# Kernel optimization log

Measured on AMD Instinct MI355X. Metric: run time of the kernel, lower is better.

The kernel has to match this reference:

```python
import jax, jax.numpy as jnp
import numpy as np

D_MODEL = 1024
D_MEMORY = 768
NUM_HEADS = 16
HEAD_DIM = D_MODEL // NUM_HEADS


def _linear_params(key, d_in, d_out):
    kw, kb = jax.random.split(key)
    bound = 1.0 / np.sqrt(d_in)
    W = jax.random.uniform(kw, (d_out, d_in), jnp.float32, -bound, bound)
    b = jax.random.uniform(kb, (d_out,), jnp.float32, -bound, bound)
    return W, b


def setup_inputs() -> dict:
    key = jax.random.key(0)
    ks = jax.random.split(key, 9)
    B, S, M = 2, 2048, 4096
    query = jax.random.normal(ks[0], (B, S, D_MODEL), jnp.float32)
    memory_keys = jax.random.normal(ks[1], (B, M, D_MEMORY), jnp.float32)
    memory_values = jax.random.normal(ks[2], (B, M, D_MEMORY), jnp.float32)
    Wq, bq = _linear_params(ks[3], D_MODEL, D_MODEL)
    Wk, bk = _linear_params(ks[4], D_MEMORY, D_MODEL)
    Wv, bv = _linear_params(ks[5], D_MEMORY, D_MODEL)
    Wo, bo = _linear_params(ks[6], D_MODEL, D_MODEL)
    Wg1, bg1 = _linear_params(ks[7], 2 * D_MODEL, D_MODEL)
    Wg2, bg2 = _linear_params(ks[8], D_MODEL, 1)
    return dict(query=query, memory_keys=memory_keys, memory_values=memory_values,
                Wq=Wq, bq=bq, Wk=Wk, bk=bk, Wv=Wv, bv=bv, Wo=Wo, bo=bo,
                Wg1=Wg1, bg1=bg1, Wg2=Wg2, bg2=bg2)


def reference(query, memory_keys, memory_values,
              Wq, bq, Wk, bk, Wv, bv, Wo, bo, Wg1, bg1, Wg2, bg2):
    B, S, _ = query.shape
    M = memory_keys.shape[1]
    H, Dh = NUM_HEADS, HEAD_DIM
    # projections (torch Linear: x @ W.T + b)
    Q = (query @ Wq.T + bq).reshape(B, S, H, Dh)
    K = (memory_keys @ Wk.T + bk).reshape(B, M, H, Dh)
    V = (memory_values @ Wv.T + bv).reshape(B, M, H, Dh)
    scale = Dh ** -0.5
    attn = jnp.einsum('bshd,bmhd->bhsm', Q, K) * scale
    attn = jax.nn.softmax(attn, axis=-1)
    retrieved = jnp.einsum('bhsm,bmhd->bshd', attn, V).reshape(B, S, H * Dh)
    retrieved = retrieved @ Wo.T + bo
    # gate: Linear -> SiLU -> Linear -> Sigmoid on [query; retrieved]
    g = jnp.concatenate([query, retrieved], axis=-1) @ Wg1.T + bg1
    g = jax.nn.silu(g)
    gate = jax.nn.sigmoid(g @ Wg2.T + bg2)  # [B,S,1]
    return query + gate * retrieved
```

## Files before the change

### kernel.cpp

```cpp
#include <hip/hip_runtime.h>

typedef __attribute__((ext_vector_type(8))) __bf16 bf16x8;
typedef __attribute__((ext_vector_type(4))) float f32x4;
typedef __attribute__((ext_vector_type(16))) float f32x16;
typedef __attribute__((ext_vector_type(8))) unsigned short u16x8;
typedef __attribute__((ext_vector_type(4))) unsigned u32x4;

__device__ __forceinline__ ushort f2bf(float x) {
    unsigned u = __builtin_bit_cast(unsigned, x);
    unsigned r = u + 0x7fffu + ((u >> 16) & 1u);
    return (ushort)(r >> 16);
}
__device__ __forceinline__ float bf2f(ushort u) {
    unsigned v = ((unsigned)u) << 16;
    return __builtin_bit_cast(float, v);
}

__device__ __forceinline__ unsigned cvtpk(float lo, float hi) {
    unsigned r;
    asm("v_cvt_pk_bf16_f32 %0, %1, %2" : "=v"(r) : "v"(lo), "v"(hi));
    return r;
}

__device__ __forceinline__ void gload16(const void* g, void* l) {
    __builtin_amdgcn_global_load_lds(
        (const __attribute__((address_space(1))) void*)g,
        (__attribute__((address_space(3))) void*)l,
        16, 0, 0);
}

#define MFMA16(a, b, cIn) __builtin_amdgcn_mfma_f32_16x16x32_bf16((a), (b), (cIn), 0, 0, 0)
#define MFMA32(a, b, cIn) __builtin_amdgcn_mfma_f32_32x32x16_bf16((a), (b), (cIn), 0, 0, 0)

__device__ __forceinline__ bf16x8 pv_frag(unsigned ua, unsigned ub, unsigned uc, unsigned ud) {
    unsigned x1 = ua, y1 = uc, x2 = ub, y2 = ud;
    asm("v_permlane32_swap_b32 %0, %1" : "+v"(x1), "+v"(y1));
    asm("v_permlane32_swap_b32 %0, %1" : "+v"(x2), "+v"(y2));
    u32x4 wv; wv[0] = x1; wv[1] = x2; wv[2] = y1; wv[3] = y2;
    return __builtin_bit_cast(bf16x8, wv);
}

__global__ __launch_bounds__(256) void cvt_kv(const float* __restrict__ a, ushort* __restrict__ ab,
                                              const float* __restrict__ bsrc, ushort* __restrict__ bb,
                                              int n4) {
    const int stride = gridDim.x * 256;
    for (int i = blockIdx.x * 256 + threadIdx.x; i < n4; i += stride) {
        float4 v = ((const float4*)a)[i];
        ushort4 o; o.x = f2bf(v.x); o.y = f2bf(v.y); o.z = f2bf(v.z); o.w = f2bf(v.w);
        ((ushort4*)ab)[i] = o;
    }
    for (int i = blockIdx.x * 256 + threadIdx.x; i < n4; i += stride) {
        float4 v = ((const float4*)bsrc)[i];
        ushort4 o; o.x = f2bf(v.x); o.y = f2bf(v.y); o.z = f2bf(v.z); o.w = f2bf(v.w);
        ((ushort4*)bb)[i] = o;
    }
}

__global__ __launch_bounds__(256) void cvt_weights(
    const float* __restrict__ s0, ushort* __restrict__ d0, int n0,
    const float* __restrict__ s1, ushort* __restrict__ d1, int n1,
    const float* __restrict__ s2, ushort* __restrict__ d2, int n2,
    const float* __restrict__ s3, ushort* __restrict__ d3, int n3,
    const float* __restrict__ s4, ushort* __restrict__ d4, int n4c) {
    const int stride = gridDim.x * 256;
    const int t0 = blockIdx.x * 256 + threadIdx.x;
#define CVT_SEG(S, D, N)                                                  \
    for (int i = t0; i < (N); i += stride) {                              \
        float4 v = ((const float4*)(S))[i];                               \
        ushort4 o; o.x = f2bf(v.x); o.y = f2bf(v.y);                      \
        o.z = f2bf(v.z); o.w = f2bf(v.w);                                 \
        ((ushort4*)(D))[i] = o;                                           \
    }
    CVT_SEG(s0, d0, n0) CVT_SEG(s1, d1, n1) CVT_SEG(s2, d2, n2)
    CVT_SEG(s3, d3, n3) CVT_SEG(s4, d4, n4c)
#undef CVT_SEG
}

__global__ __launch_bounds__(256) void cvt_query_cat(const float* __restrict__ in,
                                                     ushort* __restrict__ cat) {
    const int r = blockIdx.x, t = threadIdx.x;
    float4 v = ((const float4*)(in + (size_t)r * 1024))[t];
    ushort4 o;
    o.x = f2bf(v.x); o.y = f2bf(v.y); o.z = f2bf(v.z); o.w = f2bf(v.w);
    ((ushort4*)(cat + (size_t)r * 2048))[t] = o;
}

template<int EPI>
__global__ __launch_bounds__(256, 2) void gemm_bt(
    const ushort* __restrict__ A, int lda,
    const ushort* __restrict__ Bw, int ldb,
    const float* __restrict__ bias,
    ushort* __restrict__ o_bf, int ld0,
    float* __restrict__ o_f32,
    int K, float scale)
{
    __shared__ __align__(1024) char smem[65536];
    const int t = threadIdx.x, w = t >> 6, l = t & 63, g = l >> 4, c = l & 15;
    const int wr = w >> 1, wc = w & 1;
    const long m0 = (long)blockIdx.y * 128, n0 = (long)blockIdx.x * 128;
    const size_t ldaB = (size_t)lda * 2, ldbB = (size_t)ldb * 2;
    const int swz = (c & 7) << 4;
    const int o0 = w * 1024 + l * 16;

    auto gsrc = [&](const char* base, size_t ldB, long r0, int o) {
        const int row = o >> 7, cb = o & 127;
        return base + (size_t)(r0 + row) * ldB + (cb ^ ((row & 7) << 4));
    };
    const char* aP0 = gsrc((const char*)A, ldaB, m0, o0);
    const char* aP1 = gsrc((const char*)A, ldaB, m0, o0 + 4096);
    const char* aP2 = gsrc((const char*)A, ldaB, m0, o0 + 8192);
    const char* aP3 = gsrc((const char*)A, ldaB, m0, o0 + 12288);
    const char* bP0 = gsrc((const char*)Bw, ldbB, n0, o0);
    const char* bP1 = gsrc((const char*)Bw, ldbB, n0, o0 + 4096);
    const char* bP2 = gsrc((const char*)Bw, ldbB, n0, o0 + 8192);
    const char* bP3 = gsrc((const char*)Bw, ldbB, n0, o0 + 12288);

    const int aRd0 = (wr * 64 + c) * 128 + ((g * 16) ^ swz);
    const int aRd1 = aRd0 ^ 64;
    const int bRd0 = 32768 + (wc * 64 + c) * 128 + ((g * 16) ^ swz);
    const int bRd1 = bRd0 ^ 64;

    f32x4 acc[4][4];
#pragma unroll
    for (int i = 0; i < 4; ++i)
#pragma unroll
        for (int j = 0; j < 4; ++j) acc[i][j] = (f32x4)0.0f;

    auto stage = [&](int slot) {
        char* Ab = smem + slot * 16384;
        char* Bb = smem + 32768 + slot * 16384;
        gload16(aP0, Ab + w * 1024);
        gload16(aP1, Ab + 4096 + w * 1024);
        gload16(aP2, Ab + 8192 + w * 1024);
        gload16(aP3, Ab + 12288 + w * 1024);
        gload16(bP0, Bb + w * 1024);
        gload16(bP1, Bb + 4096 + w * 1024);
        gload16(bP2, Bb + 8192 + w * 1024);
        gload16(bP3, Bb + 12288 + w * 1024);
        aP0 += 128; aP1 += 128; aP2 += 128; aP3 += 128;
        bP0 += 128; bP1 += 128; bP2 += 128; bP3 += 128;
    };

    const int nkt = K >> 6;
    stage(0);
    for (int kt = 0; kt < nkt; ++kt) {
        const bool pf = (kt + 1 < nkt);
        if (pf) {
            stage((kt + 1) & 1);
            asm volatile("s_waitcnt vmcnt(8)" ::: "memory");
        } else {
            asm volatile("s_waitcnt vmcnt(0)" ::: "memory");
        }
        __builtin_amdgcn_s_barrier();
        const char* Ac = smem + (kt & 1) * 16384;
        const char* Bc = smem + (kt & 1) * 16384;
#pragma unroll
        for (int kf = 0; kf < 2; ++kf) {
            const int ar = kf ? aRd1 : aRd0, br = kf ? bRd1 : bRd0;
            bf16x8 af0 = *(const bf16x8*)(Ac + 0 + ar);
            bf16x8 af1 = *(const bf16x8*)(Ac + 2048 + ar);
            bf16x8 af2 = *(const bf16x8*)(Ac + 4096 + ar);
            bf16x8 af3 = *(const bf16x8*)(Ac + 6144 + ar);
            bf16x8 bf0 = *(const bf16x8*)(Bc + 0 + br);
            bf16x8 bf1 = *(const bf16x8*)(Bc + 2048 + br);
            bf16x8 bf2 = *(const bf16x8*)(Bc + 4096 + br);
            bf16x8 bf3 = *(const bf16x8*)(Bc + 6144 + br);
#pragma unroll
            for (int i = 0; i < 4; ++i) {
                const bf16x8 af = (i == 0) ? af0 : (i == 1) ? af1 : (i == 2) ? af2 : af3;
                acc[i][0] = MFMA16(af, bf0, acc[i][0]);
                acc[i][1] = MFMA16(af, bf1, acc[i][1]);
                acc[i][2] = MFMA16(af, bf2, acc[i][2]);
                acc[i][3] = MFMA16(af, bf3, acc[i][3]);
            }
        }
        if (pf) __builtin_amdgcn_s_barrier();
    }

#pragma unroll
    for (int i = 0; i < 4; ++i)
#pragma unroll
        for (int j = 0; j < 4; ++j) {
            const long col = n0 + wc * 64 + j * 16 + c;
            const float bs = bias[col];
            const long rowb = m0 + wr * 64 + i * 16 + g * 4;
            if (EPI == 1) {
                ushort4 o;
                o.x = f2bf(acc[i][j][0] + bs);
                o.y = f2bf(acc[i][j][1] + bs);
                o.z = f2bf(acc[i][j][2] + bs);
                o.w = f2bf(acc[i][j][3] + bs);
                *(ushort4*)(o_bf + col * (long)ld0 + rowb) = o;
            } else {
#pragma unroll
                for (int jj = 0; jj < 4; ++jj) {
                    const long row = rowb + jj;
                    const float v = acc[i][j][jj] + bs;
                    if (EPI == 0) {
                        o_bf[row * (long)ld0 + col] = f2bf(v * scale);
                    } else if (EPI == 2) {
                        o_f32[row * (long)ld0 + col] = v;
                        o_bf[row * 2048 + col] = f2bf(v);
                    } else {
                        const float sv = v / (1.0f + __expf(-v));
                        o_bf[row * (long)ld0 + col] = f2bf(sv);
                    }
                }
            }
        }
}

__global__ __launch_bounds__(256, 2) void attn_fwd(
    const ushort* __restrict__ qp, const ushort* __restrict__ kp,
    const ushort* __restrict__ vT, ushort* __restrict__ out)
{
    __shared__ __align__(1024) char smem[49152];
    const int t = threadIdx.x, w = t >> 6, l = t & 63;
    const int c = l & 31, hi = l >> 5;
    const int b = blockIdx.z, h = blockIdx.y;
    const int s0w = blockIdx.x * 128 + w * 32;

    const size_t qbase = ((size_t)b * 2048 + s0w + c) * 1024 + h * 64 + hi * 8;
    const bf16x8 qf0 = *(const bf16x8*)(qp + qbase);
    const bf16x8 qf1 = *(const bf16x8*)(qp + qbase + 16);
    const bf16x8 qf2 = *(const bf16x8*)(qp + qbase + 32);
    const bf16x8 qf3 = *(const bf16x8*)(qp + qbase + 48);

    const u16x8 ones_u = (u16x8)(ushort)0x3F80;
    const bf16x8 ones = __builtin_bit_cast(bf16x8, ones_u);

    f32x16 oacc0 = (f32x16)0.0f, oacc1 = (f32x16)0.0f, lacc = (f32x16)0.0f;

    const int swz = (c & 7) << 4;
    const int rb = c * 128 + ((hi * 16) ^ swz);

    const char* kpB = (const char*)kp + (size_t)b * 4096 * 2048 + h * 128;
    const char* vTB = (const char*)vT + (size_t)h * 64 * 16384 + (size_t)b * 4096 * 2;
    const int o0 = w * 1024 + l * 16;
    auto mksrc = [&](const char* base, size_t ldB, int o) {
        const int row = o >> 7, cb = o & 127;
        return base + (size_t)row * ldB + (cb ^ ((row & 7) << 4));
    };
    const char* kg0 = mksrc(kpB, 2048, o0);
    const char* kg1 = mksrc(kpB, 2048, o0 + 4096);
    const char* vg0 = mksrc(vTB, 16384, o0);
    const char* vg1 = mksrc(vTB, 16384, o0 + 4096);

    auto stage = [&](int stK) {
        gload16(kg0, smem + stK + w * 1024);
        gload16(kg1, smem + stK + 4096 + w * 1024);
        gload16(vg0, smem + 24576 + stK + w * 1024);
        gload16(vg1, smem + 24576 + stK + 4096 + w * 1024);
        kg0 += 131072; kg1 += 131072; vg0 += 128; vg1 += 128;
    };

    stage(0);
    stage(8192);
    asm volatile("s_waitcnt vmcnt(4)" ::: "memory");
    __builtin_amdgcn_s_barrier();

    int rdK = 0, stK = 16384;
    for (int ti = 0; ti < 64; ++ti) {
        const bool pf = (ti < 62);
        if (pf) {
            stage(stK);
            stK = (stK == 16384) ? 0 : stK + 8192;
        }
        const char* Ksc = smem + rdK;
        const char* Vsc = smem + 24576 + rdK;

        f32x16 s0v = (f32x16)0.0f, s1v = (f32x16)0.0f;
        {
            bf16x8 k0;
            k0 = *(const bf16x8*)(Ksc + (rb ^ 0));         s0v = MFMA32(k0, qf0, s0v);
            k0 = *(const bf16x8*)(Ksc + (rb ^ 32));        s0v = MFMA32(k0, qf1, s0v);
            k0 = *(const bf16x8*)(Ksc + (rb ^ 64));        s0v = MFMA32(k0, qf2, s0v);
            k0 = *(const bf16x8*)(Ksc + (rb ^ 96));        s0v = MFMA32(k0, qf3, s0v);
            k0 = *(const bf16x8*)(Ksc + 4096 + (rb ^ 0));  s1v = MFMA32(k0, qf0, s1v);
            k0 = *(const bf16x8*)(Ksc + 4096 + (rb ^ 32)); s1v = MFMA32(k0, qf1, s1v);
            k0 = *(const bf16x8*)(Ksc + 4096 + (rb ^ 64)); s1v = MFMA32(k0, qf2, s1v);
            k0 = *(const bf16x8*)(Ksc + 4096 + (rb ^ 96)); s1v = MFMA32(k0, qf3, s1v);
        }

#define PV_HALF(SV, MB0, MB1)                                                   \
        {                                                                       \
            const float p0 = exp2f(SV[0]),  p1 = exp2f(SV[1]);                  \
            const float p2 = exp2f(SV[2]),  p3 = exp2f(SV[3]);                  \
            const float p4 = exp2f(SV[4]),  p5 = exp2f(SV[5]);                  \
            const float p6 = exp2f(SV[6]),  p7 = exp2f(SV[7]);                  \
            const float p8 = exp2f(SV[8]),  p9 = exp2f(SV[9]);                  \
            const float pa_ = exp2f(SV[10]), pb_ = exp2f(SV[11]);               \
            const float pc_ = exp2f(SV[12]), pd_ = exp2f(SV[13]);               \
            const float pe_ = exp2f(SV[14]), pf_ = exp2f(SV[15]);               \
            const unsigned u0 = cvtpk(p0, p1), u1 = cvtpk(p2, p3);              \
            const unsigned u2 = cvtpk(p4, p5), u3 = cvtpk(p6, p7);              \
            const unsigned u4 = cvtpk(p8, p9), u5 = cvtpk(pa_, pb_);            \
            const unsigned u6 = cvtpk(pc_, pd_), u7 = cvtpk(pe_, pf_);          \
            const bf16x8 paA = pv_frag(u0, u1, u2, u3);        \
            const bf16x8 paB = pv_frag(u4, u5, u6, u7);        \
            bf16x8 vb;                                                          \
            lacc = MFMA32(paA, ones, lacc);                                     \
            vb = *(const bf16x8*)(Vsc + (rb ^ (MB0 * 32)));                     \
            oacc0 = MFMA32(paA, vb, oacc0);                                     \
            vb = *(const bf16x8*)(Vsc + 4096 + (rb ^ (MB0 * 32)));              \
            oacc1 = MFMA32(paA, vb, oacc1);                                     \
            lacc = MFMA32(paB, ones, lacc);                                     \
            vb = *(const bf16x8*)(Vsc + (rb ^ (MB1 * 32)));                     \
            oacc0 = MFMA32(paB, vb, oacc0);                                     \
            vb = *(const bf16x8*)(Vsc + 4096 + (rb ^ (MB1 * 32)));              \
            oacc1 = MFMA32(paB, vb, oacc1);                                     \
        }
        PV_HALF(s0v, 0, 1)
        PV_HALF(s1v, 2, 3)
#undef PV_HALF

        rdK = (rdK == 16384) ? 0 : rdK + 8192;
        if (pf) asm volatile("s_waitcnt vmcnt(4)" ::: "memory");
        else    asm volatile("s_waitcnt vmcnt(0)" ::: "memory");
        __builtin_amdgcn_s_barrier();
    }

    const size_t obase = ((size_t)b * 2048 + s0w) * 1024 + h * 64 + c;
#pragma unroll
    for (int r = 0; r < 16; ++r) {
        const int q = (r & 3) + 8 * (r >> 2) + 4 * hi;
        const float rinv = 1.0f / lacc[r];
        out[obase + (size_t)q * 1024]      = f2bf(oacc0[r] * rinv);
        out[obase + (size_t)q * 1024 + 32] = f2bf(oacc1[r] * rinv);
    }
}

__global__ __launch_bounds__(256) void gate_out_k(
    const ushort* __restrict__ gs, const float* __restrict__ Wg2,
    const float* __restrict__ bg2, const float* __restrict__ query,
    const float* __restrict__ retr, float* __restrict__ out)
{
    const int r = blockIdx.x, t = threadIdx.x, w = t >> 6, l = t & 63;
    ushort4 gv = ((const ushort4*)(gs + (size_t)r * 1024))[t];
    float4 wv = ((const float4*)Wg2)[t];
    float p = bf2f(gv.x) * wv.x + bf2f(gv.y) * wv.y + bf2f(gv.z) * wv.z + bf2f(gv.w) * wv.w;
    for (int m = 1; m < 64; m <<= 1) p += __shfl_xor(p, m);
    __shared__ float red[4];
    if (l == 0) red[w] = p;
    __syncthreads();
    const float dot = red[0] + red[1] + red[2] + red[3] + bg2[0];
    const float gate = 1.0f / (1.0f + __expf(-dot));
    float4 q = ((const float4*)(query + (size_t)r * 1024))[t];
    float4 rt = ((const float4*)(retr + (size_t)r * 1024))[t];
    float4 o;
    o.x = q.x + gate * rt.x; o.y = q.y + gate * rt.y;
    o.z = q.z + gate * rt.z; o.w = q.w + gate * rt.w;
    ((float4*)(out + (size_t)r * 1024))[t] = o;
}

extern "C" void kernel_launch(void* const* d_in, const int* in_sizes, int n_in,
                              void* d_out, int out_size, void* d_ws, size_t ws_size,
                              hipStream_t stream) {
    const float* query = (const float*)d_in[0];
    const float* mkeys = (const float*)d_in[1];
    const float* mvals = (const float*)d_in[2];
    const float* Wq  = (const float*)d_in[3];
    const float* bq  = (const float*)d_in[4];
    const float* Wk  = (const float*)d_in[5];
    const float* bk  = (const float*)d_in[6];
    const float* Wv  = (const float*)d_in[7];
    const float* bv  = (const float*)d_in[8];
    const float* Wo  = (const float*)d_in[9];
    const float* bo  = (const float*)d_in[10];
    const float* Wg1 = (const float*)d_in[11];
    const float* bg1 = (const float*)d_in[12];
    const float* Wg2 = (const float*)d_in[13];
    const float* bg2 = (const float*)d_in[14];
    float* outF = (float*)d_out;

    char* ws = (char*)d_ws;
    size_t off = 0;
    auto take = [&](size_t bytes) { char* p = ws + off; off += (bytes + 255) & ~(size_t)255; return p; };
    ushort* cat    = (ushort*)take((size_t)4096 * 2048 * 2);
    ushort* mkbf   = (ushort*)take((size_t)8192 * 768 * 2);
    ushort* mvbf   = (ushort*)take((size_t)8192 * 768 * 2);
    ushort* wqbf   = (ushort*)take((size_t)1024 * 1024 * 2);
    ushort* wkbf   = (ushort*)take((size_t)1024 * 768 * 2);
    ushort* wvbf   = (ushort*)take((size_t)1024 * 768 * 2);
    ushort* wobf   = (ushort*)take((size_t)1024 * 1024 * 2);
    ushort* wg1bf  = (ushort*)take((size_t)1024 * 2048 * 2);
    ushort* qproj  = (ushort*)take((size_t)4096 * 1024 * 2);
    ushort* kproj  = (ushort*)take((size_t)8192 * 1024 * 2);
    ushort* vprojT = (ushort*)take((size_t)1024 * 8192 * 2);
    ushort* attno  = (ushort*)take((size_t)4096 * 1024 * 2);
    float*  retro  = (float*)take((size_t)4096 * 1024 * 4);
    ushort* gsilu  = (ushort*)take((size_t)4096 * 1024 * 2);

    cvt_query_cat<<<4096, 256, 0, stream>>>(query, cat);
    cvt_kv<<<2048, 256, 0, stream>>>(mkeys, mkbf, mvals, mvbf, 8192 * 768 / 4);
    cvt_weights<<<1024, 256, 0, stream>>>(Wq, wqbf, 1024 * 1024 / 4,
                                          Wk, wkbf, 1024 * 768 / 4,
                                          Wv, wvbf, 1024 * 768 / 4,
                                          Wo, wobf, 1024 * 1024 / 4,
                                          Wg1, wg1bf, 1024 * 2048 / 4);

    const float qscale = 0.125f * 1.44269504088896340736f;
    gemm_bt<0><<<dim3(8, 32), 256, 0, stream>>>(cat, 2048, wqbf, 1024, bq, qproj, 1024, nullptr, 1024, qscale);
    gemm_bt<0><<<dim3(8, 64), 256, 0, stream>>>(mkbf, 768, wkbf, 768, bk, kproj, 1024, nullptr, 768, 1.0f);
    gemm_bt<1><<<dim3(8, 64), 256, 0, stream>>>(mvbf, 768, wvbf, 768, bv, vprojT, 8192, nullptr, 768, 1.0f);
    attn_fwd<<<dim3(16, 16, 2), 256, 0, stream>>>(qproj, kproj, vprojT, attno);
    gemm_bt<2><<<dim3(8, 32), 256, 0, stream>>>(attno, 1024, wobf, 1024, bo, cat + 1024, 1024, retro, 1024, 1.0f);
    gemm_bt<3><<<dim3(8, 32), 256, 0, stream>>>(cat, 2048, wg1bf, 2048, bg1, gsilu, 1024, nullptr, 2048, 1.0f);
    gate_out_k<<<4096, 256, 0, stream>>>(gsilu, Wg2, bg2, query, retro, outF);
}
```

Baseline: 369.8 us.

## Batch projection GEMMs into one grouped launch and split gate GEMM by K

New measurement: 349.7 us. 1.06x faster.

```diff
diff --git a/kernel.cpp b/kernel.cpp
--- a/kernel.cpp
+++ b/kernel.cpp
@@ -21,6 +21,8 @@
     asm("v_cvt_pk_bf16_f32 %0, %1, %2" : "=v"(r) : "v"(lo), "v"(hi));
     return r;
 }
+
+#define E2(x) __builtin_amdgcn_exp2f(x)
 
 __device__ __forceinline__ void gload16(const void* g, void* l) {
     __builtin_amdgcn_global_load_lds(
@@ -85,20 +87,28 @@
     ((ushort4*)(cat + (size_t)r * 2048))[t] = o;
 }
 
-template<int EPI>
-__global__ __launch_bounds__(256, 2) void gemm_bt(
-    const ushort* __restrict__ A, int lda,
-    const ushort* __restrict__ Bw, int ldb,
-    const float* __restrict__ bias,
-    ushort* __restrict__ o_bf, int ld0,
-    float* __restrict__ o_f32,
-    int K, float scale)
-{
+struct GemmDesc {
+    const ushort* A; const ushort* Bw; const float* bias;
+    ushort* obf; float* of32;
+    int lda, ldb, ld0, nkt, epi, tiles_m, base;
+    float scale;
+};
+
+__global__ __launch_bounds__(256, 2) void gemm_fused(GemmDesc d0, GemmDesc d1,
+                                                     GemmDesc d2, GemmDesc d3) {
     __shared__ __align__(1024) char smem[65536];
     const int t = threadIdx.x, w = t >> 6, l = t & 63, g = l >> 4, c = l & 15;
     const int wr = w >> 1, wc = w & 1;
-    const long m0 = (long)blockIdx.y * 128, n0 = (long)blockIdx.x * 128;
-    const size_t ldaB = (size_t)lda * 2, ldbB = (size_t)ldb * 2;
+    const int bid0 = blockIdx.x;
+    const int bid = (bid0 & 7) * 192 + (bid0 >> 3);
+    GemmDesc d = d3;
+    if (bid < d1.base) d = d0;
+    else if (bid < d2.base) d = d1;
+    else if (bid < d3.base) d = d2;
+    const int tix = bid - d.base;
+    const int tm = tix % d.tiles_m, tn = tix / d.tiles_m;
+    const long m0 = (long)tm * 128, n0 = (long)tn * 128;
+    const size_t ldaB = (size_t)d.lda * 2, ldbB = (size_t)d.ldb * 2;
     const int swz = (c & 7) << 4;
     const int o0 = w * 1024 + l * 16;
 
@@ -106,14 +116,14 @@
         const int row = o >> 7, cb = o & 127;
         return base + (size_t)(r0 + row) * ldB + (cb ^ ((row & 7) << 4));
     };
-    const char* aP0 = gsrc((const char*)A, ldaB, m0, o0);
-    const char* aP1 = gsrc((const char*)A, ldaB, m0, o0 + 4096);
-    const char* aP2 = gsrc((const char*)A, ldaB, m0, o0 + 8192);
-    const char* aP3 = gsrc((const char*)A, ldaB, m0, o0 + 12288);
-    const char* bP0 = gsrc((const char*)Bw, ldbB, n0, o0);
-    const char* bP1 = gsrc((const char*)Bw, ldbB, n0, o0 + 4096);
-    const char* bP2 = gsrc((const char*)Bw, ldbB, n0, o0 + 8192);
-    const char* bP3 = gsrc((const char*)Bw, ldbB, n0, o0 + 12288);
+    const char* aP0 = gsrc((const char*)d.A, ldaB, m0, o0);
+    const char* aP1 = gsrc((const char*)d.A, ldaB, m0, o0 + 4096);
+    const char* aP2 = gsrc((const char*)d.A, ldaB, m0, o0 + 8192);
+    const char* aP3 = gsrc((const char*)d.A, ldaB, m0, o0 + 12288);
+    const char* bP0 = gsrc((const char*)d.Bw, ldbB, n0, o0);
+    const char* bP1 = gsrc((const char*)d.Bw, ldbB, n0, o0 + 4096);
+    const char* bP2 = gsrc((const char*)d.Bw, ldbB, n0, o0 + 8192);
+    const char* bP3 = gsrc((const char*)d.Bw, ldbB, n0, o0 + 12288);
 
     const int aRd0 = (wr * 64 + c) * 128 + ((g * 16) ^ swz);
     const int aRd1 = aRd0 ^ 64;
@@ -141,7 +151,7 @@
         bP0 += 128; bP1 += 128; bP2 += 128; bP3 += 128;
     };
 
-    const int nkt = K >> 6;
+    const int nkt = d.nkt;
     stage(0);
     for (int kt = 0; kt < nkt; ++kt) {
         const bool pf = (kt + 1 < nkt);
@@ -182,29 +192,130 @@
 #pragma unroll
         for (int j = 0; j < 4; ++j) {
             const long col = n0 + wc * 64 + j * 16 + c;
-            const float bs = bias[col];
             const long rowb = m0 + wr * 64 + i * 16 + g * 4;
-            if (EPI == 1) {
+            if (d.epi == 1) {
+                const float bs = d.bias[col];
                 ushort4 o;
                 o.x = f2bf(acc[i][j][0] + bs);
                 o.y = f2bf(acc[i][j][1] + bs);
                 o.z = f2bf(acc[i][j][2] + bs);
                 o.w = f2bf(acc[i][j][3] + bs);
-                *(ushort4*)(o_bf + col * (long)ld0 + rowb) = o;
+                *(ushort4*)(d.obf + col * (long)d.ld0 + rowb) = o;
+            } else if (d.epi == 4) {
+#pragma unroll
+                for (int jj = 0; jj < 4; ++jj)
+                    d.of32[(rowb + jj) * (long)d.ld0 + col] = acc[i][j][jj];
             } else {
-#pragma unroll
-                for (int jj = 0; jj < 4; ++jj) {
-                    const long row = rowb + jj;
+                const float bs = d.bias[col];
+#pragma unroll
+                for (int jj = 0; jj < 4; ++jj)
+                    d.obf[(rowb + jj) * (long)d.ld0 + col] = f2bf((acc[i][j][jj] + bs) * d.scale);
+            }
+        }
+}
+
+template<int EPI>
+__global__ __launch_bounds__(256, 2) void gemm_tail(
+    const ushort* __restrict__ A, int lda,
+    const ushort* __restrict__ Bw, int ldb,
+    const float* __restrict__ bias,
+    ushort* __restrict__ o_bf, int ld0,
+    float* __restrict__ o_f32, int K) {
+    __shared__ __align__(1024) char smem[49152];
+    const int t = threadIdx.x, w = t >> 6, l = t & 63, g = l >> 4, c = l & 15;
+    const int wr = w >> 1, wc = w & 1;
+    const long m0 = (long)blockIdx.y * 64, n0 = (long)blockIdx.x * 128;
+    const size_t ldaB = (size_t)lda * 2, ldbB = (size_t)ldb * 2;
+    const int swz = (c & 7) << 4;
+    const int o0 = w * 1024 + l * 16;
+
+    auto gsrc = [&](const char* base, size_t ldB, long r0, int o) {
+        const int row = o >> 7, cb = o & 127;
+        return base + (size_t)(r0 + row) * ldB + (cb ^ ((row & 7) << 4));
+    };
+    const char* aP0 = gsrc((const char*)A, ldaB, m0, o0);
+    const char* aP1 = gsrc((const char*)A, ldaB, m0, o0 + 4096);
+    const char* bP0 = gsrc((const char*)Bw, ldbB, n0, o0);
+    const char* bP1 = gsrc((const char*)Bw, ldbB, n0, o0 + 4096);
+    const char* bP2 = gsrc((const char*)Bw, ldbB, n0, o0 + 8192);
+    const char* bP3 = gsrc((const char*)Bw, ldbB, n0, o0 + 12288);
+
+    const int aRd0 = (wr * 32 + c) * 128 + ((g * 16) ^ swz);
+    const int aRd1 = aRd0 ^ 64;
+    const int bRd0 = 16384 + (wc * 64 + c) * 128 + ((g * 16) ^ swz);
+    const int bRd1 = bRd0 ^ 64;
+
+    f32x4 acc[2][4];
+#pragma unroll
+    for (int i = 0; i < 2; ++i)
+#pragma unroll
+        for (int j = 0; j < 4; ++j) acc[i][j] = (f32x4)0.0f;
+
+    auto stage = [&](int slot) {
+        char* Ab = smem + slot * 8192;
+        char* Bb = smem + 16384 + slot * 16384;
+        gload16(aP0, Ab + w * 1024);
+        gload16(aP1, Ab + 4096 + w * 1024);
+        gload16(bP0, Bb + w * 1024);
+        gload16(bP1, Bb + 4096 + w * 1024);
+        gload16(bP2, Bb + 8192 + w * 1024);
+        gload16(bP3, Bb + 12288 + w * 1024);
+        aP0 += 128; aP1 += 128;
+        bP0 += 128; bP1 += 128; bP2 += 128; bP3 += 128;
+    };
+
+    const int nkt = K >> 6;
+    stage(0);
+    for (int kt = 0; kt < nkt; ++kt) {
+        const bool pf = (kt + 1 < nkt);
+        if (pf) {
+            stage((kt + 1) & 1);
+            asm volatile("s_waitcnt vmcnt(6)" ::: "memory");
+        } else {
+            asm volatile("s_waitcnt vmcnt(0)" ::: "memory");
+        }
+        __builtin_amdgcn_s_barrier();
+        const char* Ac = smem + (kt & 1) * 8192;
+        const char* Bc = smem + (kt & 1) * 16384;
+#pragma unroll
+        for (int kf = 0; kf < 2; ++kf) {
+            const int ar = kf ? aRd1 : aRd0, br = kf ? bRd1 : bRd0;
+            bf16x8 af0 = *(const bf16x8*)(Ac + 0 + ar);
+            bf16x8 af1 = *(const bf16x8*)(Ac + 2048 + ar);
+            bf16x8 bf0 = *(const bf16x8*)(Bc + 0 + br);
+            bf16x8 bf1 = *(const bf16x8*)(Bc + 2048 + br);
+            bf16x8 bf2 = *(const bf16x8*)(Bc + 4096 + br);
+            bf16x8 bf3 = *(const bf16x8*)(Bc + 6144 + br);
+            acc[0][0] = MFMA16(af0, bf0, acc[0][0]);
+            acc[0][1] = MFMA16(af0, bf1, acc[0][1]);
+            acc[0][2] = MFMA16(af0, bf2, acc[0][2]);
+            acc[0][3] = MFMA16(af0, bf3, acc[0][3]);
+            acc[1][0] = MFMA16(af1, bf0, acc[1][0]);
+            acc[1][1] = MFMA16(af1, bf1, acc[1][1]);
+            acc[1][2] = MFMA16(af1, bf2, acc[1][2]);
+            acc[1][3] = MFMA16(af1, bf3, acc[1][3]);
+        }
+        if (pf) __builtin_amdgcn_s_barrier();
+    }
+
+#pragma unroll
+    for (int i = 0; i < 2; ++i)
+#pragma unroll
+        for (int j = 0; j < 4; ++j) {
+            const long col = n0 + wc * 64 + j * 16 + c;
+            const float bs = bias[col];
+            const long rowb = m0 + wr * 32 + i * 16 + g * 4;
+#pragma unroll
+            for (int jj = 0; jj < 4; ++jj) {
+                const long row = rowb + jj;
+                if (EPI == 2) {
                     const float v = acc[i][j][jj] + bs;
-                    if (EPI == 0) {
-                        o_bf[row * (long)ld0 + col] = f2bf(v * scale);
-                    } else if (EPI == 2) {
-                        o_f32[row * (long)ld0 + col] = v;
-                        o_bf[row * 2048 + col] = f2bf(v);
-                    } else {
-                        const float sv = v / (1.0f + __expf(-v));
-                        o_bf[row * (long)ld0 + col] = f2bf(sv);
-                    }
+                    o_f32[row * (long)ld0 + col] = v;
+                    o_bf[row * 2048 + col] = f2bf(v);
+                } else {
+                    const float v = acc[i][j][jj] + bs + o_f32[row * (long)ld0 + col];
+                    const float sv = v / (1.0f + __expf(-v));
+                    o_bf[row * (long)ld0 + col] = f2bf(sv);
                 }
             }
         }
@@ -270,6 +381,7 @@
         const char* Vsc = smem + 24576 + rdK;
 
         f32x16 s0v = (f32x16)0.0f, s1v = (f32x16)0.0f;
+        __builtin_amdgcn_s_setprio(1);
         {
             bf16x8 k0;
             k0 = *(const bf16x8*)(Ksc + (rb ^ 0));         s0v = MFMA32(k0, qf0, s0v);
@@ -281,24 +393,26 @@
             k0 = *(const bf16x8*)(Ksc + 4096 + (rb ^ 64)); s1v = MFMA32(k0, qf2, s1v);
             k0 = *(const bf16x8*)(Ksc + 4096 + (rb ^ 96)); s1v = MFMA32(k0, qf3, s1v);
         }
+        __builtin_amdgcn_s_setprio(0);
 
 #define PV_HALF(SV, MB0, MB1)                                                   \
         {                                                                       \
-            const float p0 = exp2f(SV[0]),  p1 = exp2f(SV[1]);                  \
-            const float p2 = exp2f(SV[2]),  p3 = exp2f(SV[3]);                  \
-            const float p4 = exp2f(SV[4]),  p5 = exp2f(SV[5]);                  \
-            const float p6 = exp2f(SV[6]),  p7 = exp2f(SV[7]);                  \
-            const float p8 = exp2f(SV[8]),  p9 = exp2f(SV[9]);                  \
-            const float pa_ = exp2f(SV[10]), pb_ = exp2f(SV[11]);               \
-            const float pc_ = exp2f(SV[12]), pd_ = exp2f(SV[13]);               \
-            const float pe_ = exp2f(SV[14]), pf_ = exp2f(SV[15]);               \
+            const float p0 = E2(SV[0]),  p1 = E2(SV[1]);                        \
+            const float p2 = E2(SV[2]),  p3 = E2(SV[3]);                        \
+            const float p4 = E2(SV[4]),  p5 = E2(SV[5]);                        \
+            const float p6 = E2(SV[6]),  p7 = E2(SV[7]);                        \
+            const float p8 = E2(SV[8]),  p9 = E2(SV[9]);                        \
+            const float pa_ = E2(SV[10]), pb_ = E2(SV[11]);                     \
+            const float pc_ = E2(SV[12]), pd_ = E2(SV[13]);                     \
+            const float pe_ = E2(SV[14]), pf_ = E2(SV[15]);                     \
             const unsigned u0 = cvtpk(p0, p1), u1 = cvtpk(p2, p3);              \
             const unsigned u2 = cvtpk(p4, p5), u3 = cvtpk(p6, p7);              \
             const unsigned u4 = cvtpk(p8, p9), u5 = cvtpk(pa_, pb_);            \
             const unsigned u6 = cvtpk(pc_, pd_), u7 = cvtpk(pe_, pf_);          \
-            const bf16x8 paA = pv_frag(u0, u1, u2, u3);        \
-            const bf16x8 paB = pv_frag(u4, u5, u6, u7);        \
+            const bf16x8 paA = pv_frag(u0, u1, u2, u3);                         \
+            const bf16x8 paB = pv_frag(u4, u5, u6, u7);                         \
             bf16x8 vb;                                                          \
+            __builtin_amdgcn_s_setprio(1);                                      \
             lacc = MFMA32(paA, ones, lacc);                                     \
             vb = *(const bf16x8*)(Vsc + (rb ^ (MB0 * 32)));                     \
             oacc0 = MFMA32(paA, vb, oacc0);                                     \
@@ -309,6 +423,7 @@
             oacc0 = MFMA32(paB, vb, oacc0);                                     \
             vb = *(const bf16x8*)(Vsc + 4096 + (rb ^ (MB1 * 32)));              \
             oacc1 = MFMA32(paB, vb, oacc1);                                     \
+            __builtin_amdgcn_s_setprio(0);                                      \
         }
         PV_HALF(s0v, 0, 1)
         PV_HALF(s1v, 2, 3)
@@ -390,6 +505,7 @@
     ushort* attno  = (ushort*)take((size_t)4096 * 1024 * 2);
     float*  retro  = (float*)take((size_t)4096 * 1024 * 4);
     ushort* gsilu  = (ushort*)take((size_t)4096 * 1024 * 2);
+    float*  gpre   = (float*)take((size_t)4096 * 1024 * 4);
 
     cvt_query_cat<<<4096, 256, 0, stream>>>(query, cat);
     cvt_kv<<<2048, 256, 0, stream>>>(mkeys, mkbf, mvals, mvbf, 8192 * 768 / 4);
@@ -400,11 +516,17 @@
                                           Wg1, wg1bf, 1024 * 2048 / 4);
 
     const float qscale = 0.125f * 1.44269504088896340736f;
-    gemm_bt<0><<<dim3(8, 32), 256, 0, stream>>>(cat, 2048, wqbf, 1024, bq, qproj, 1024, nullptr, 1024, qscale);
-    gemm_bt<0><<<dim3(8, 64), 256, 0, stream>>>(mkbf, 768, wkbf, 768, bk, kproj, 1024, nullptr, 768, 1.0f);
-    gemm_bt<1><<<dim3(8, 64), 256, 0, stream>>>(mvbf, 768, wvbf, 768, bv, vprojT, 8192, nullptr, 768, 1.0f);
+    GemmDesc dQ { cat,   wqbf,          bq,  qproj,  nullptr, 2048, 1024, 1024, 16, 0, 32,    0, qscale };
+    GemmDesc dK { mkbf,  wkbf,          bk,  kproj,  nullptr,  768,  768, 1024, 12, 0, 64,  256, 1.0f };
+    GemmDesc dV { mvbf,  wvbf,          bv,  vprojT, nullptr,  768,  768, 8192, 12, 1, 64,  768, 1.0f };
+    GemmDesc dG { cat,   wg1bf,         bg1, nullptr, gpre,   2048, 2048, 1024, 16, 4, 32, 1280, 1.0f };
+    gemm_fused<<<1536, 256, 0, stream>>>(dQ, dK, dV, dG);
+
     attn_fwd<<<dim3(16, 16, 2), 256, 0, stream>>>(qproj, kproj, vprojT, attno);
-    gemm_bt<2><<<dim3(8, 32), 256, 0, stream>>>(attno, 1024, wobf, 1024, bo, cat + 1024, 1024, retro, 1024, 1.0f);
-    gemm_bt<3><<<dim3(8, 32), 256, 0, stream>>>(cat, 2048, wg1bf, 2048, bg1, gsilu, 1024, nullptr, 2048, 1.0f);
+
+    gemm_tail<2><<<dim3(8, 64), 256, 0, stream>>>(attno, 1024, wobf, 1024, bo,
+                                                  cat + 1024, 1024, retro, 1024);
+    gemm_tail<5><<<dim3(8, 64), 256, 0, stream>>>(cat + 1024, 2048, wg1bf + 1024, 2048, bg1,
+                                                  gsilu, 1024, gpre, 1024);
     gate_out_k<<<4096, 256, 0, stream>>>(gsilu, Wg2, bg2, query, retro, outF);
 }
```
